# Optimization experiments

Hardware: AMD Instinct MI355X
Metric: run time of the kernel (lower is better)

Reference implementation:

```python
import jax, jax.numpy as jnp
import numpy as np
import math

V = 32000      # vocab_size
D = 1024       # hidden_dims
T_MAX = 1024   # max_txt_len
L = 4          # n_layers
H = 8          # heads (fixed in CausalMHA)
HD = D // H
B, T = 2, 1024
EPS = 1e-5


def setup_inputs() -> dict:
    key = jax.random.key(0)
    ks = jax.random.split(key, 20)
    s = 0.02
    inp = {
        "x": jax.random.randint(ks[0], (B, T), 0, V, dtype=jnp.int64) if jax.config.read("jax_enable_x64") else jax.random.randint(ks[0], (B, T), 0, V, dtype=jnp.int32),
        "tok_emb": jax.random.normal(ks[1], (V, D), jnp.float32) * s,
        "pos_emb": jax.random.normal(ks[2], (1, T_MAX, D), jnp.float32) * s,
        "ln1_g": jnp.ones((L, D), jnp.float32),
        "ln1_b": jnp.zeros((L, D), jnp.float32),
        "wqkv": jax.random.normal(ks[3], (L, D, 3 * D), jnp.float32) * s,
        "bqkv": jnp.zeros((L, 3 * D), jnp.float32),
        "wo": jax.random.normal(ks[4], (L, D, D), jnp.float32) * s,
        "bo": jnp.zeros((L, D), jnp.float32),
        "ln2_g": jnp.ones((L, D), jnp.float32),
        "ln2_b": jnp.zeros((L, D), jnp.float32),
        "wfc": jax.random.normal(ks[5], (L, D, 4 * D), jnp.float32) * s,   # no bias
        "wfc2": jax.random.normal(ks[6], (L, 4 * D, D), jnp.float32) * s,  # no bias
        "fn_g": jnp.ones((D,), jnp.float32),
        "fn_b": jnp.zeros((D,), jnp.float32),
        "wout": jax.random.normal(ks[7], (D, V), jnp.float32) * s,
        "bout": jnp.zeros((V,), jnp.float32),
    }
    return inp


def _ln(x, g, b):
    mu = jnp.mean(x, axis=-1, keepdims=True)
    var = jnp.var(x, axis=-1, keepdims=True)
    return (x - mu) * jax.lax.rsqrt(var + EPS) * g + b


def _attn(xn, wqkv_l, bqkv_l, wo_l, bo_l):
    Bb, Tt, _ = xn.shape
    qkv = xn @ wqkv_l + bqkv_l                      # [B,T,3D]
    q, k, v = jnp.split(qkv, 3, axis=-1)
    q = q.reshape(Bb, Tt, H, HD)
    k = k.reshape(Bb, Tt, H, HD)
    v = v.reshape(Bb, Tt, H, HD)
    scores = jnp.einsum("bqhd,bkhd->bhqk", q, k) / math.sqrt(HD)
    mask = jnp.triu(jnp.ones((Tt, Tt), bool), k=1)   # True above diagonal
    scores = jnp.where(mask, jnp.float32(-jnp.inf), scores)
    att = jax.nn.softmax(scores, axis=-1)
    out = jnp.einsum("bhqk,bkhd->bqhd", att, v).reshape(Bb, Tt, D)
    return out @ wo_l + bo_l


def reference(x, tok_emb, pos_emb, ln1_g, ln1_b, wqkv, bqkv, wo, bo,
              ln2_g, ln2_b, wfc, wfc2, fn_g, fn_b, wout, bout):
    Tt = x.shape[1]
    h = tok_emb[x] + pos_emb[:, :Tt, :]              # [B,T,D]
    for i in range(L):
        h = h + _attn(_ln(h, ln1_g[i], ln1_b[i]), wqkv[i], bqkv[i], wo[i], bo[i])
        hn = _ln(h, ln2_g[i], ln2_b[i])
        h = h + jax.nn.gelu(hn @ wfc[i], approximate=False) @ wfc2[i]
    h = _ln(h, fn_g, fn_b)
    return h @ wout + bout                           # [B,T,V] logits
```

## Files before the change

### kernel.cpp

```cpp
#include <hip/hip_runtime.h>
#include <math.h>
#include <stdint.h>

#define D_  1024
#define T_  1024
#define H_  8
#define HD_ 128
#define L_  4
#define V_  32000
#define M_  2048

typedef __attribute__((ext_vector_type(4))) float f32x4;
typedef __attribute__((ext_vector_type(4))) short s16x4;
typedef __attribute__((ext_vector_type(8))) short s16x8;
typedef unsigned short u16;

__device__ __forceinline__ u16 f2bf(float f) {
  union { float f; uint32_t u; } c; c.f = f;
  uint32_t r = c.u + 0x7fffu + ((c.u >> 16) & 1u);
  return (u16)(r >> 16);
}
__device__ __forceinline__ float bf2f(u16 h) {
  union { uint32_t u; float f; } c; c.u = ((uint32_t)h) << 16;
  return c.f;
}
__device__ __forceinline__ float gelu_f(float x) {
  return 0.5f * x * (1.0f + erff(x * 0.70710678118654752f));
}

__device__ __forceinline__ void gload16(const u16* g, u16* l) {
  __builtin_amdgcn_global_load_lds(
      (const __attribute__((address_space(1))) void*)(uintptr_t)g,
      (__attribute__((address_space(3))) void*)(uint32_t)(uintptr_t)l,
      16, 0, 0);
}

__device__ __forceinline__ void convT_f32_tile(const float* __restrict__ in,
                                               u16* __restrict__ out,
                                               int ldin, int ldout,
                                               int c0, int r0,
                                               u16 (*tile)[72])
{
  const int t = threadIdx.x;
  const int rr = t >> 2, cs = (t & 3) << 4;
  u16 tmp[16];
  const float* p = in + (size_t)(r0 + rr) * ldin + c0 + cs;
#pragma unroll
  for (int q = 0; q < 4; ++q) {
    f32x4 v = *(const f32x4*)(p + q * 4);
#pragma unroll
    for (int j = 0; j < 4; ++j) tmp[q * 4 + j] = f2bf(v[j]);
  }
  *(s16x8*)&tile[rr][cs]     = *(const s16x8*)tmp;
  *(s16x8*)&tile[rr][cs + 8] = *(const s16x8*)(tmp + 8);
  __syncthreads();
  const int cr = t >> 2, rs = (t & 3) << 4;
  u16 o[16];
#pragma unroll
  for (int j = 0; j < 16; ++j) o[j] = tile[rs + j][cr];
  u16* op = out + (size_t)(c0 + cr) * ldout + r0 + rs;
  *(s16x8*)op       = *(const s16x8*)o;
  *(s16x8*)(op + 8) = *(const s16x8*)(o + 8);
}

template<int INF32>
__global__ __launch_bounds__(256)
void convT_kernel(const void* __restrict__ inv, u16* __restrict__ out,
                  int ldin, int ldout, long inZ, long outZ)
{
  __shared__ __align__(16) u16 tile[64][72];
  const int c0 = blockIdx.x << 6, r0 = blockIdx.y << 6;
  if (INF32) {
    convT_f32_tile((const float*)inv + (size_t)blockIdx.z * inZ,
                   out + (size_t)blockIdx.z * outZ, ldin, ldout, c0, r0, tile);
    return;
  }
  const int t = threadIdx.x;
  const int rr = t >> 2, cs = (t & 3) << 4;
  const u16* in = (const u16*)inv + (size_t)blockIdx.z * inZ;
  const u16* p = in + (size_t)(r0 + rr) * ldin + c0 + cs;
  s16x8 v0 = *(const s16x8*)(p);
  s16x8 v1 = *(const s16x8*)(p + 8);
  *(s16x8*)&tile[rr][cs]     = v0;
  *(s16x8*)&tile[rr][cs + 8] = v1;
  __syncthreads();
  const int cr = t >> 2, rs = (t & 3) << 4;
  u16 o[16];
#pragma unroll
  for (int j = 0; j < 16; ++j) o[j] = tile[rs + j][cr];
  u16* op = out + (size_t)blockIdx.z * outZ + (size_t)(c0 + cr) * ldout + r0 + rs;
  *(s16x8*)op       = *(const s16x8*)o;
  *(s16x8*)(op + 8) = *(const s16x8*)(o + 8);
}

__global__ __launch_bounds__(256)
void conv4_kernel(const float* __restrict__ wqkv_l, const float* __restrict__ wo_l,
                  const float* __restrict__ wfc_l, const float* __restrict__ wfc2_l,
                  u16* __restrict__ Wq, u16* __restrict__ Wo,
                  u16* __restrict__ Wf1, u16* __restrict__ Wf2)
{
  __shared__ __align__(16) u16 tile[64][72];
  int f = blockIdx.x;
  if (f < 768) {
    convT_f32_tile(wqkv_l, Wq, 3 * D_, D_, (f % 48) << 6, (f / 48) << 6, tile);
  } else if (f < 1024) {
    f -= 768;
    convT_f32_tile(wo_l, Wo, D_, D_, (f & 15) << 6, (f >> 4) << 6, tile);
  } else if (f < 2048) {
    f -= 1024;
    convT_f32_tile(wfc_l, Wf1, 4 * D_, D_, (f & 63) << 6, (f >> 6) << 6, tile);
  } else {
    f -= 2048;
    convT_f32_tile(wfc2_l, Wf2, D_, 4 * D_, (f & 15) << 6, (f >> 4) << 6, tile);
  }
}

template<int TM, int ACT, int BIAS, int OUT>
__device__ __forceinline__
void gemm2_body(const u16* __restrict__ A, const u16* __restrict__ Bw,
                const float* __restrict__ bias, const float* __restrict__ res,
                void* __restrict__ Cv,
                int K, int lda, int ldb, int ldc, float scale,
                int bx, int by)
{
  constexpr int WN  = (TM == 128) ? 2 : 4;
  constexpr int WNW = 128 / WN;
  constexpr int NJ  = WNW / 16;
  constexpr int AR  = TM / 64;

  const int m0 = bx * TM, n0 = by * 128;
  const int ktiles = K >> 5;

  __shared__ __align__(16) u16 As[2][TM * 32];
  __shared__ __align__(16) u16 Bs[2][128 * 32];

  const int tid = threadIdx.x, lane = tid & 63, wave = tid >> 6;
  const int wm = wave / WN, wn = wave % WN;
  const int l15 = lane & 15, l4 = lane >> 4;
  const int srow = lane >> 2, scol = (lane & 3) << 3;

  f32x4 acc[4][NJ];
  const f32x4 z4 = {0.f, 0.f, 0.f, 0.f};
#pragma unroll
  for (int i = 0; i < 4; ++i)
#pragma unroll
    for (int j = 0; j < NJ; ++j) acc[i][j] = z4;

  auto stage = [&](int kt, int buf) {
    const int kc = (kt << 5) + scol;
#pragma unroll
    for (int r = 0; r < AR; ++r) {
      const int row = r * 64 + wave * 16;
      gload16(A + (size_t)(m0 + row + srow) * lda + kc, &As[buf][row * 32]);
    }
#pragma unroll
    for (int r = 0; r < 2; ++r) {
      const int row = r * 64 + wave * 16;
      gload16(Bw + (size_t)(n0 + row + srow) * ldb + kc, &Bs[buf][row * 32]);
    }
  };

  stage(0, 0);
  __syncthreads();

  for (int kt = 0; kt < ktiles; ++kt) {
    const int buf = kt & 1;
    if (kt + 1 < ktiles) stage(kt + 1, buf ^ 1);
    const u16* ap = &As[buf][(wm * 64 + l15) * 32 + (l4 << 3)];
    const u16* bp = &Bs[buf][(wn * WNW + l15) * 32 + (l4 << 3)];
    s16x8 af[4], bf[NJ];
#pragma unroll
    for (int i = 0; i < 4; ++i) af[i] = *(const s16x8*)(ap + i * (16 * 32));
#pragma unroll
    for (int j = 0; j < NJ; ++j) bf[j] = *(const s16x8*)(bp + j * (16 * 32));
#pragma unroll
    for (int i = 0; i < 4; ++i)
#pragma unroll
      for (int j = 0; j < NJ; ++j)
        acc[i][j] = __builtin_amdgcn_mfma_f32_16x16x32_bf16(af[i], bf[j], acc[i][j], 0, 0, 0);
    __syncthreads();
  }

  float* Cf = (float*)Cv;
  u16*   Ch = (u16*)Cv;
#pragma unroll
  for (int i = 0; i < 4; ++i) {
    const int row0 = m0 + wm * 64 + i * 16 + l4 * 4;
#pragma unroll
    for (int j = 0; j < NJ; ++j) {
      const int col = n0 + wn * WNW + j * 16 + l15;
      const float bv = BIAS ? bias[col] : 0.0f;
#pragma unroll
      for (int r = 0; r < 4; ++r) {
        float v = acc[i][j][r] * scale + bv;
        if (ACT) v = gelu_f(v);
        const size_t idx = (size_t)(row0 + r) * ldc + col;
        if (OUT == 0)      Ch[idx] = f2bf(v);
        else if (OUT == 1) Cf[idx] = v;
        else               Cf[idx] = v + res[idx];
      }
    }
  }
}

__device__ __forceinline__ int2 swz2d() {
  const int gx = gridDim.x, gy = gridDim.y;
  int flat = blockIdx.y * gx + blockIdx.x;
  const int nwg = gx * gy;
  int swz = (flat & 7) * (nwg >> 3) + (flat >> 3);
  return make_int2(swz % gx, swz / gx);
}

__global__ __launch_bounds__(256)
void gemm_qkv(const u16* A, const u16* Bw, const float* bias, void* Cv) {
  int2 b = swz2d();
  gemm2_body<128, 0, 1, 0>(A, Bw, bias, nullptr, Cv, D_, D_, D_, 3 * D_, 1.0f, b.x, b.y);
}
__global__ __launch_bounds__(256)
void gemm_wo(const u16* A, const u16* Bw, const float* bias, const float* res,
             void* Cv) {
  int2 b = swz2d();
  gemm2_body<64, 0, 1, 2>(A, Bw, bias, res, Cv, D_, D_, D_, D_, 1.0f, b.x, b.y);
}

template<int OUT, int ACT>
__device__ __forceinline__
void gemm8n_body(const u16* __restrict__ A, int lda,
                 const u16* __restrict__ Bw, int ldb,
                 void* __restrict__ Cv, int ldc, int bx, int by)
{
  const int m0 = bx << 8, n0 = by << 7;

  __shared__ __align__(16) u16 lds[49152];

  const int tid = threadIdx.x, lane = tid & 63, wave = tid >> 6;
  const int wm = wave >> 1, wn = wave & 1;
  const int l15 = lane & 15, l4 = lane >> 4;

  f32x4 acc[4][4];
  const f32x4 z4 = {0.f, 0.f, 0.f, 0.f};
#pragma unroll
  for (int i = 0; i < 4; ++i)
#pragma unroll
    for (int j = 0; j < 4; ++j) acc[i][j] = z4;

  auto stgA = [&](int buf, int kt, int kh) {
    kt = (kt < 15) ? kt : 15;
    const int slot = buf * 24576 + kh * 8192;
#pragma unroll
    for (int r = 0; r < 2; ++r) {
      const int u = r * 512 + (wave << 6) + lane;
      const int rw = u >> 2, ks = u & 3;
      const int ksw = ks ^ ((rw >> 1) & 3);
      gload16(A + (size_t)(m0 + rw) * lda + (kt << 6) + (kh << 5) + (ksw << 3),
              &lds[slot + r * 4096 + (wave << 9)]);
    }
  };
  auto stgB = [&](int buf, int kt, int kh) {
    kt = (kt < 15) ? kt : 15;
    const int slot = buf * 24576 + 16384 + kh * 4096;
    const int u = (wave << 6) + lane;
    const int rw = u >> 2, ks = u & 3;
    const int ksw = ks ^ ((rw >> 1) & 3);
    gload16(Bw + (size_t)(n0 + rw) * ldb + (kt << 6) + (kh << 5) + (ksw << 3),
            &lds[slot + (wave << 9)]);
  };

  s16x8 af[4], bfr[4];

#define LDABN(bb, kk)                                                         \
  {                                                                           \
    _Pragma("unroll") for (int f = 0; f < 4; ++f) {                           \
      const int rw = wm * 64 + f * 16 + l15;                                  \
      af[f] = *(const s16x8*)&lds[(bb) + (kk) * 8192 + rw * 32 +              \
                                  ((l4 ^ ((rw >> 1) & 3)) << 3)];             \
    }                                                                         \
    _Pragma("unroll") for (int f = 0; f < 4; ++f) {                           \
      const int rn = wn * 64 + f * 16 + l15;                                  \
      bfr[f] = *(const s16x8*)&lds[(bb) + 16384 + (kk) * 4096 + rn * 32 +     \
                                   ((l4 ^ ((rn >> 1) & 3)) << 3)];            \
    }                                                                         \
  }
#define MFMAN()                                                               \
  {                                                                           \
    __builtin_amdgcn_s_barrier();                                             \
    asm volatile("s_waitcnt lgkmcnt(0)" ::: "memory");                        \
    __builtin_amdgcn_sched_barrier(0);                                        \
    __builtin_amdgcn_s_setprio(1);                                            \
    _Pragma("unroll") for (int f = 0; f < 4; ++f)                             \
      _Pragma("unroll") for (int nf = 0; nf < 4; ++nf)                        \
        acc[f][nf] = __builtin_amdgcn_mfma_f32_16x16x32_bf16(                 \
            af[f], bfr[nf], acc[f][nf], 0, 0, 0);                             \
    __builtin_amdgcn_s_setprio(0);                                            \
  }
#define BARN() __builtin_amdgcn_s_barrier()
#define VM6()  asm volatile("s_waitcnt vmcnt(6)" ::: "memory")

  stgA(0, 0, 0); stgB(0, 0, 0);
  stgA(0, 0, 1); stgB(0, 0, 1);
  stgA(1, 1, 0); stgB(1, 1, 0);
  VM6();
  BARN();

  for (int i = 0; i < 8; ++i) {
    const int t = 2 * i;
    LDABN(0, 0);
    stgA(1, t + 1, 1); stgB(1, t + 1, 1);
    MFMAN(); VM6(); BARN();
    LDABN(0, 1);
    stgA(0, t + 2, 0); stgB(0, t + 2, 0);
    MFMAN(); VM6(); BARN();
    LDABN(24576, 0);
    stgA(0, t + 2, 1); stgB(0, t + 2, 1);
    MFMAN(); VM6(); BARN();
    LDABN(24576, 1);
    stgA(1, t + 3, 0); stgB(1, t + 3, 0);
    MFMAN(); VM6(); BARN();
  }
#undef LDABN
#undef MFMAN
#undef BARN
#undef VM6

  float* Cf = (float*)Cv;
  u16*   Ch = (u16*)Cv;
#pragma unroll
  for (int mf = 0; mf < 4; ++mf) {
    const int row0 = m0 + wm * 64 + mf * 16 + l4 * 4;
#pragma unroll
    for (int nf = 0; nf < 4; ++nf) {
      const int col = n0 + wn * 64 + nf * 16 + l15;
#pragma unroll
      for (int r = 0; r < 4; ++r) {
        float v = acc[mf][nf][r];
        if (ACT) v = gelu_f(v);
        const size_t idx = (size_t)(row0 + r) * ldc + col;
        if (OUT == 0) Ch[idx] = f2bf(v);
        else          Cf[idx] = v;
      }
    }
  }
}

__global__ __launch_bounds__(512, 1)
void gemm8n_fc1(const u16* A, const u16* Bw, void* Cv) {
  int flat = blockIdx.x;
  int swz = (flat & 7) * 32 + (flat >> 3);
  gemm8n_body<0, 1>(A, 1024, Bw, 1024, Cv, 4096, swz & 7, swz >> 3);
}
__global__ __launch_bounds__(512, 1)
void gemm8n_fc2(const u16* A, const u16* Bw, float* P) {
  int flat = blockIdx.x;
  int swz = (flat & 7) * 32 + (flat >> 3);
  const int bx = swz & 7, by = (swz >> 3) & 7, z = swz >> 6;
  gemm8n_body<1, 0>(A + z * 1024, 4096, Bw + z * 1024, 4096,
                    P + (size_t)z * M_ * D_, 1024, bx, by);
}

__global__ __launch_bounds__(512, 2)
void gemm8_logits(const u16* __restrict__ A, const u16* __restrict__ Bw,
                  const float* __restrict__ bias, float* __restrict__ C)
{
  int flat = blockIdx.x;
  int swz = (flat & 7) * 125 + (flat >> 3);
  const int bx = swz & 7;
  const int by = swz >> 3;
  const int m0 = bx << 8, n0 = by << 8;

  __shared__ __align__(16) u16 lds[65536];

  const int tid = threadIdx.x, lane = tid & 63, wave = tid >> 6;
  const int wm = wave >> 2, wn = wave & 3;
  const int l15 = lane & 15, l4 = lane >> 4;

  f32x4 acc[8][4];
  const f32x4 z4 = {0.f, 0.f, 0.f, 0.f};
#pragma unroll
  for (int i = 0; i < 8; ++i)
#pragma unroll
    for (int j = 0; j < 4; ++j) acc[i][j] = z4;

  auto stg = [&](const u16* G, int rowbase, int slot, int kt, int kh) {
    kt = (kt < 15) ? kt : 15;
#pragma unroll
    for (int r = 0; r < 2; ++r) {
      const int u = r * 512 + (wave << 6) + lane;
      const int rw = u >> 2, ks = u & 3;
      const int ksw = ks ^ ((rw >> 1) & 3);
      const u16* src = G + (size_t)(rowbase + rw) * 1024 + (kt << 6) + (kh << 5) + (ksw << 3);
      gload16(src, &lds[slot + r * 4096 + (wave << 9)]);
    }
  };

  s16x8 af[4], bfr[4];

#define LDA4(bb, kk, mh)                                                      \
  {                                                                           \
    _Pragma("unroll") for (int f = 0; f < 4; ++f) {                           \
      const int rw = wm * 128 + (mh) * 64 + f * 16 + l15;                     \
      af[f] = *(const s16x8*)&lds[(bb) + (kk) * 8192 + rw * 32 +              \
                                  ((l4 ^ ((rw >> 1) & 3)) << 3)];             \
    }                                                                         \
  }
#define LDB4(bb, kk)                                                          \
  {                                                                           \
    _Pragma("unroll") for (int f = 0; f < 4; ++f) {                           \
      const int rn = wn * 64 + f * 16 + l15;                                  \
      bfr[f] = *(const s16x8*)&lds[(bb) + 16384 + (kk) * 8192 + rn * 32 +     \
                                   ((l4 ^ ((rn >> 1) & 3)) << 3)];            \
    }                                                                         \
  }
#define MFMA16(mh)                                                            \
  {                                                                           \
    __builtin_amdgcn_s_barrier();                                             \
    asm volatile("s_waitcnt lgkmcnt(0)" ::: "memory");                        \
    __builtin_amdgcn_sched_barrier(0);                                        \
    __builtin_amdgcn_s_setprio(1);                                            \
    _Pragma("unroll") for (int f = 0; f < 4; ++f)                             \
      _Pragma("unroll") for (int nf = 0; nf < 4; ++nf)                        \
        acc[(mh) * 4 + f][nf] = __builtin_amdgcn_mfma_f32_16x16x32_bf16(      \
            af[f], bfr[nf], acc[(mh) * 4 + f][nf], 0, 0, 0);                  \
    __builtin_amdgcn_s_setprio(0);                                            \
  }
#define BAR() __builtin_amdgcn_s_barrier()
#define VM4() asm volatile("s_waitcnt vmcnt(4)" ::: "memory")

  stg(A,  m0, 0,             0, 0);
  stg(Bw, n0, 16384,         0, 0);
  stg(A,  m0, 8192,          0, 1);
  stg(Bw, n0, 16384 + 8192,  0, 1);
  stg(A,  m0, 32768,         1, 0);
  stg(Bw, n0, 32768 + 16384, 1, 0);
  VM4();
  BAR();

  for (int i = 0; i < 8; ++i) {
    const int t = 2 * i;
    LDA4(0, 0, 0); LDB4(0, 0);
    stg(A, m0, 32768 + 8192, t + 1, 1);
    MFMA16(0); BAR();
    LDA4(0, 0, 1);
    stg(Bw, n0, 32768 + 24576, t + 1, 1);
    MFMA16(1); BAR();
    LDA4(0, 1, 0); LDB4(0, 1);
    stg(A, m0, 0, t + 2, 0);
    MFMA16(0); BAR();
    LDA4(0, 1, 1);
    stg(Bw, n0, 16384, t + 2, 0);
    MFMA16(1); VM4(); BAR();
    LDA4(32768, 0, 0); LDB4(32768, 0);
    stg(A, m0, 8192, t + 2, 1);
    MFMA16(0); BAR();
    LDA4(32768, 0, 1);
    stg(Bw, n0, 16384 + 8192, t + 2, 1);
    MFMA16(1); BAR();
    LDA4(32768, 1, 0); LDB4(32768, 1);
    stg(A, m0, 32768, t + 3, 0);
    MFMA16(0); BAR();
    LDA4(32768, 1, 1);
    stg(Bw, n0, 32768 + 16384, t + 3, 0);
    MFMA16(1); VM4(); BAR();
  }
#undef LDA4
#undef LDB4
#undef MFMA16
#undef BAR
#undef VM4

  float bv[4];
#pragma unroll
  for (int nf = 0; nf < 4; ++nf) bv[nf] = bias[n0 + wn * 64 + nf * 16 + l15];
#pragma unroll
  for (int mf = 0; mf < 8; ++mf) {
    const int row0 = m0 + wm * 128 + mf * 16 + l4 * 4;
#pragma unroll
    for (int nf = 0; nf < 4; ++nf) {
      const int col = n0 + wn * 64 + nf * 16 + l15;
#pragma unroll
      for (int r = 0; r < 4; ++r)
        C[(size_t)(row0 + r) * V_ + col] = acc[mf][nf][r] + bv[nf];
    }
  }
}

__global__ __launch_bounds__(256)
void flash_attn(const u16* __restrict__ qkv, const u16* __restrict__ Vt,
                u16* __restrict__ xo)
{
  const int qb = 15 - blockIdx.x;
  const int z  = blockIdx.y;
  const int b  = z >> 3, hh = z & 7;

  __shared__ __align__(16) u16 Ks[64 * 128];
  __shared__ __align__(16) u16 Vs[128 * 64];
  __shared__ __align__(16) u16 Ps[64 * 80];

  const int tid = threadIdx.x, lane = tid & 63, w = tid >> 6;
  const int l15 = lane & 15, l4 = lane >> 4;
  const float iscale = 0.08838834764831845f;

  const int qrow = qb * 64 + w * 16 + l15;
  const u16* qptr = qkv + ((size_t)(b * T_) + qrow) * (3 * D_) + hh * HD_;

  s16x8 bQ[4];
#pragma unroll
  for (int ks = 0; ks < 4; ++ks)
    bQ[ks] = *(const s16x8*)(qptr + ks * 32 + l4 * 8);

  f32x4 O[8];
#pragma unroll
  for (int i = 0; i < 8; ++i) O[i] = {0.f, 0.f, 0.f, 0.f};
  float m_run = -1e30f, l_run = 0.f;

  const int ntiles = qb + 1;
  for (int kt = 0; kt < ntiles; ++kt) {
    __syncthreads();
    {
      const int r = tid >> 2, c = (tid & 3) << 5;
      const u16* src = qkv + ((size_t)(b * T_) + kt * 64 + r) * (3 * D_) + D_ + hh * HD_ + c;
#pragma unroll
      for (int u = 0; u < 4; ++u) {
        s16x8 v = *(const s16x8*)(src + u * 8);
        const int dblk = (c >> 3) + u;
        *(s16x8*)&Ks[r * 128 + ((dblk ^ (r & 7)) << 3)] = v;
      }
      const int d = tid >> 1, kc0 = (tid & 1) << 5;
      const u16* vsrc = Vt + ((size_t)z * HD_ + d) * T_ + kt * 64 + kc0;
#pragma unroll
      for (int u = 0; u < 4; ++u) {
        s16x8 v = *(const s16x8*)(vsrc + u * 8);
        const int kblk = (kc0 >> 3) + u;
        *(s16x8*)&Vs[d * 64 + ((kblk ^ (d & 7)) << 3)] = v;
      }
    }
    __syncthreads();

    f32x4 st[4];
#pragma unroll
    for (int mf = 0; mf < 4; ++mf) st[mf] = {0.f, 0.f, 0.f, 0.f};
#pragma unroll
    for (int ks = 0; ks < 4; ++ks) {
      s16x8 aK[4];
#pragma unroll
      for (int mf = 0; mf < 4; ++mf) {
        const int r = mf * 16 + l15;
        aK[mf] = *(const s16x8*)&Ks[r * 128 + ((((ks << 2) + l4) ^ (r & 7)) << 3)];
      }
#pragma unroll
      for (int mf = 0; mf < 4; ++mf)
        st[mf] = __builtin_amdgcn_mfma_f32_16x16x32_bf16(aK[mf], bQ[ks], st[mf], 0, 0, 0);
    }

    const bool diag = (kt == qb);
    float sv[16];
    float mx = -1e30f;
#pragma unroll
    for (int mf = 0; mf < 4; ++mf)
#pragma unroll
      for (int r = 0; r < 4; ++r) {
        float s = st[mf][r] * iscale;
        if (diag) {
          const int k = kt * 64 + mf * 16 + l4 * 4 + r;
          if (k > qrow) s = -1e30f;
        }
        sv[mf * 4 + r] = s;
        mx = fmaxf(mx, s);
      }
    mx = fmaxf(mx, __shfl_xor(mx, 16));
    mx = fmaxf(mx, __shfl_xor(mx, 32));
    const float m_new = fmaxf(m_run, mx);
    const float sc_old = __expf(m_run - m_new);
    float psum = 0.f;
    u16 pb[16];
#pragma unroll
    for (int j = 0; j < 16; ++j) {
      const float p = __expf(sv[j] - m_new);
      psum += p;
      pb[j] = f2bf(p);
    }
    psum += __shfl_xor(psum, 16);
    psum += __shfl_xor(psum, 32);
    l_run = l_run * sc_old + psum;
    m_run = m_new;

    float scr[4];
#pragma unroll
    for (int r = 0; r < 4; ++r) scr[r] = __shfl(sc_old, l4 * 4 + r);
#pragma unroll
    for (int df = 0; df < 8; ++df)
#pragma unroll
      for (int r = 0; r < 4; ++r) O[df][r] *= scr[r];

    {
      const int row = w * 16 + l15;
#pragma unroll
      for (int j = 0; j < 16; ++j) {
        const int k = (j >> 2) * 16 + l4 * 4 + (j & 3);
        Ps[row * 80 + (((k >> 3) ^ (l15 & 7)) << 3) + (k & 7)] = pb[j];
      }
    }

#pragma unroll
    for (int kc = 0; kc < 2; ++kc) {
      const int prow = w * 16 + l15;
      s16x8 aP = *(const s16x8*)&Ps[prow * 80 + ((((kc << 2) + l4) ^ (l15 & 7)) << 3)];
#pragma unroll
      for (int df = 0; df < 8; ++df) {
        const int d = df * 16 + l15;
        s16x8 bV = *(const s16x8*)&Vs[d * 64 + ((((kc << 2) + l4) ^ (d & 7)) << 3)];
        O[df] = __builtin_amdgcn_mfma_f32_16x16x32_bf16(aP, bV, O[df], 0, 0, 0);
      }
    }
  }

  const float inv_l = 1.0f / l_run;
  float invr[4];
#pragma unroll
  for (int r = 0; r < 4; ++r) invr[r] = __shfl(inv_l, l4 * 4 + r);
#pragma unroll
  for (int df = 0; df < 8; ++df)
#pragma unroll
    for (int r = 0; r < 4; ++r) {
      const int row = qb * 64 + w * 16 + l4 * 4 + r;
      xo[((size_t)(b * T_) + row) * D_ + hh * HD_ + df * 16 + l15] =
          f2bf(O[df][r] * invr[r]);
    }
}

__global__ __launch_bounds__(256)
void ln_red(float* __restrict__ hbuf, const float* __restrict__ P,
            const float* __restrict__ g, const float* __restrict__ b,
            u16* __restrict__ y, int red)
{
  __shared__ float red_s[8];
  const int row = blockIdx.x, tid = threadIdx.x;
  const size_t i = (size_t)row * D_ + tid * 4;
  f32x4 v = *(const f32x4*)&hbuf[i];
  if (red) {
#pragma unroll
    for (int zp = 0; zp < 4; ++zp) {
      f32x4 p = *(const f32x4*)&P[(size_t)zp * M_ * D_ + i];
      v[0] += p[0]; v[1] += p[1]; v[2] += p[2]; v[3] += p[3];
    }
    *(f32x4*)&hbuf[i] = v;
  }
  float s  = v[0] + v[1] + v[2] + v[3];
  float s2 = v[0]*v[0] + v[1]*v[1] + v[2]*v[2] + v[3]*v[3];
#pragma unroll
  for (int off = 32; off > 0; off >>= 1) {
    s  += __shfl_xor(s, off);
    s2 += __shfl_xor(s2, off);
  }
  if ((tid & 63) == 0) { red_s[tid >> 6] = s; red_s[4 + (tid >> 6)] = s2; }
  __syncthreads();
  s  = red_s[0] + red_s[1] + red_s[2] + red_s[3];
  s2 = red_s[4] + red_s[5] + red_s[6] + red_s[7];
  const float mean = s * (1.0f / D_);
  const float var  = s2 * (1.0f / D_) - mean * mean;
  const float rs   = rsqrtf(var + 1e-5f);
  f32x4 gg = *(const f32x4*)&g[tid * 4];
  f32x4 bb = *(const f32x4*)&b[tid * 4];
  u16 o[4];
#pragma unroll
  for (int j = 0; j < 4; ++j) o[j] = f2bf((v[j] - mean) * rs * gg[j] + bb[j]);
  *(s16x4*)&y[i] = *(const s16x4*)o;
}

__global__ __launch_bounds__(256)
void embed_kernel(const int* __restrict__ x, const float* __restrict__ tok,
                  const float* __restrict__ pos, float* __restrict__ h)
{
  const int row = blockIdx.x, tid = threadIdx.x;
  const int t = row & (T_ - 1);
  const int id = x[row];
  f32x4 a = *(const f32x4*)&tok[(size_t)id * D_ + tid * 4];
  f32x4 p = *(const f32x4*)&pos[(size_t)t * D_ + tid * 4];
  f32x4 o = {a[0] + p[0], a[1] + p[1], a[2] + p[2], a[3] + p[3]};
  *(f32x4*)&h[(size_t)row * D_ + tid * 4] = o;
}

extern "C" void kernel_launch(void* const* d_in, const int* in_sizes, int n_in,
                              void* d_out, int out_size, void* d_ws, size_t ws_size,
                              hipStream_t stream)
{
  (void)in_sizes; (void)n_in; (void)out_size; (void)ws_size;
  const int*   x     = (const int*)  d_in[0];
  const float* tok   = (const float*)d_in[1];
  const float* pos   = (const float*)d_in[2];
  const float* ln1_g = (const float*)d_in[3];
  const float* ln1_b = (const float*)d_in[4];
  const float* wqkv  = (const float*)d_in[5];
  const float* bqkv  = (const float*)d_in[6];
  const float* wo    = (const float*)d_in[7];
  const float* bo    = (const float*)d_in[8];
  const float* ln2_g = (const float*)d_in[9];
  const float* ln2_b = (const float*)d_in[10];
  const float* wfc   = (const float*)d_in[11];
  const float* wfc2  = (const float*)d_in[12];
  const float* fn_g  = (const float*)d_in[13];
  const float* fn_b  = (const float*)d_in[14];
  const float* wout  = (const float*)d_in[15];
  const float* bout  = (const float*)d_in[16];
  float* out = (float*)d_out;

  float* h  = (float*)d_ws;
  u16* xn   = (u16*)(h + (size_t)M_ * D_);
  u16* Wq   = xn  + (size_t)M_ * D_;
  u16* Wo   = Wq  + (size_t)3 * D_ * D_;
  u16* Wf1  = Wo  + (size_t)D_ * D_;
  u16* Wf2  = Wf1 + (size_t)4 * D_ * D_;
  u16* qkv  = Wf2 + (size_t)4 * D_ * D_;
  u16* Vt   = qkv + (size_t)M_ * 3 * D_;
  u16* S    = Vt  + (size_t)2 * T_ * D_;
  float* P  = (float*)(S + (size_t)M_ * 4 * D_);
  u16* WoutT = Wq;

  embed_kernel<<<M_, 256, 0, stream>>>(x, tok, pos, h);

  for (int l = 0; l < L_; ++l) {
    conv4_kernel<<<3072, 256, 0, stream>>>(
        wqkv + (size_t)l * D_ * 3 * D_, wo + (size_t)l * D_ * D_,
        wfc + (size_t)l * D_ * 4 * D_, wfc2 + (size_t)l * 4 * D_ * D_,
        Wq, Wo, Wf1, Wf2);

    ln_red<<<M_, 256, 0, stream>>>(h, P, ln1_g + l * D_, ln1_b + l * D_, xn,
                                   l > 0 ? 1 : 0);
    gemm_qkv<<<dim3(16, 24), 256, 0, stream>>>(xn, Wq, bqkv + l * 3 * D_, qkv);
    convT_kernel<0><<<dim3(16, 16, 2), 256, 0, stream>>>(
        qkv + 2 * D_, Vt, 3 * D_, T_, (long)T_ * 3 * D_, (long)T_ * D_);
    flash_attn<<<dim3(16, 16), 256, 0, stream>>>(qkv, Vt, xn);
    gemm_wo<<<dim3(32, 8), 256, 0, stream>>>(xn, Wo, bo + l * D_, h, h);
    ln_red<<<M_, 256, 0, stream>>>(h, P, ln2_g + l * D_, ln2_b + l * D_, xn, 0);
    gemm8n_fc1<<<256, 512, 0, stream>>>(xn, Wf1, S);
    gemm8n_fc2<<<256, 512, 0, stream>>>(S, Wf2, P);
  }

  ln_red<<<M_, 256, 0, stream>>>(h, P, fn_g, fn_b, xn, 1);
  convT_kernel<1><<<dim3(500, 16, 1), 256, 0, stream>>>(
      wout, WoutT, V_, D_, 0, 0);
  gemm8_logits<<<1000, 512, 0, stream>>>(xn, WoutT, bout, out);
}
```

Before: 895.1 us.

## Fuse layernorm into weight-conversion launches and halve flash-attention query tiles

New measurement: 880.8 us. About the same (-1.6%).

```diff
diff --git a/kernel.cpp b/kernel.cpp
--- a/kernel.cpp
+++ b/kernel.cpp
@@ -63,22 +63,53 @@
   *(s16x8*)(op + 8) = *(const s16x8*)(o + 8);
 }
 
-template<int INF32>
+__device__ __forceinline__
+void ln_row_body(int row, float* __restrict__ hbuf, const float* __restrict__ P,
+                 const float* __restrict__ g, const float* __restrict__ b,
+                 u16* __restrict__ y, int red, float* red_s)
+{
+  const int tid = threadIdx.x;
+  const size_t i = (size_t)row * D_ + tid * 4;
+  f32x4 v = *(const f32x4*)&hbuf[i];
+  if (red) {
+#pragma unroll
+    for (int zp = 0; zp < 4; ++zp) {
+      f32x4 p = *(const f32x4*)&P[(size_t)zp * M_ * D_ + i];
+      v[0] += p[0]; v[1] += p[1]; v[2] += p[2]; v[3] += p[3];
+    }
+    *(f32x4*)&hbuf[i] = v;
+  }
+  float s  = v[0] + v[1] + v[2] + v[3];
+  float s2 = v[0]*v[0] + v[1]*v[1] + v[2]*v[2] + v[3]*v[3];
+#pragma unroll
+  for (int off = 32; off > 0; off >>= 1) {
+    s  += __shfl_xor(s, off);
+    s2 += __shfl_xor(s2, off);
+  }
+  if ((tid & 63) == 0) { red_s[tid >> 6] = s; red_s[4 + (tid >> 6)] = s2; }
+  __syncthreads();
+  s  = red_s[0] + red_s[1] + red_s[2] + red_s[3];
+  s2 = red_s[4] + red_s[5] + red_s[6] + red_s[7];
+  const float mean = s * (1.0f / D_);
+  const float var  = s2 * (1.0f / D_) - mean * mean;
+  const float rs   = rsqrtf(var + 1e-5f);
+  f32x4 gg = *(const f32x4*)&g[tid * 4];
+  f32x4 bb = *(const f32x4*)&b[tid * 4];
+  u16 o[4];
+#pragma unroll
+  for (int j = 0; j < 4; ++j) o[j] = f2bf((v[j] - mean) * rs * gg[j] + bb[j]);
+  *(s16x4*)&y[i] = *(const s16x4*)o;
+}
+
 __global__ __launch_bounds__(256)
-void convT_kernel(const void* __restrict__ inv, u16* __restrict__ out,
-                  int ldin, int ldout, long inZ, long outZ)
+void convT_bf16(const u16* __restrict__ in, u16* __restrict__ out,
+                int ldin, int ldout, long inZ, long outZ)
 {
   __shared__ __align__(16) u16 tile[64][72];
   const int c0 = blockIdx.x << 6, r0 = blockIdx.y << 6;
-  if (INF32) {
-    convT_f32_tile((const float*)inv + (size_t)blockIdx.z * inZ,
-                   out + (size_t)blockIdx.z * outZ, ldin, ldout, c0, r0, tile);
-    return;
-  }
   const int t = threadIdx.x;
   const int rr = t >> 2, cs = (t & 3) << 4;
-  const u16* in = (const u16*)inv + (size_t)blockIdx.z * inZ;
-  const u16* p = in + (size_t)(r0 + rr) * ldin + c0 + cs;
+  const u16* p = in + (size_t)blockIdx.z * inZ + (size_t)(r0 + rr) * ldin + c0 + cs;
   s16x8 v0 = *(const s16x8*)(p);
   s16x8 v1 = *(const s16x8*)(p + 8);
   *(s16x8*)&tile[rr][cs]     = v0;
@@ -94,13 +125,18 @@
 }
 
 __global__ __launch_bounds__(256)
-void conv4_kernel(const float* __restrict__ wqkv_l, const float* __restrict__ wo_l,
-                  const float* __restrict__ wfc_l, const float* __restrict__ wfc2_l,
-                  u16* __restrict__ Wq, u16* __restrict__ Wo,
-                  u16* __restrict__ Wf1, u16* __restrict__ Wf2)
+void conv4ln_kernel(const float* __restrict__ wqkv_l, const float* __restrict__ wo_l,
+                    const float* __restrict__ wfc_l, const float* __restrict__ wfc2_l,
+                    u16* __restrict__ Wq, u16* __restrict__ Wo,
+                    u16* __restrict__ Wf1, u16* __restrict__ Wf2,
+                    float* __restrict__ hbuf, const float* __restrict__ P,
+                    const float* __restrict__ g, const float* __restrict__ b,
+                    u16* __restrict__ y, int red)
 {
   __shared__ __align__(16) u16 tile[64][72];
   int f = blockIdx.x;
+  if (f < 2048) { ln_row_body(f, hbuf, P, g, b, y, red, (float*)tile); return; }
+  f -= 2048;
   if (f < 768) {
     convT_f32_tile(wqkv_l, Wq, 3 * D_, D_, (f % 48) << 6, (f / 48) << 6, tile);
   } else if (f < 1024) {
@@ -113,6 +149,19 @@
     f -= 2048;
     convT_f32_tile(wfc2_l, Wf2, D_, 4 * D_, (f & 15) << 6, (f >> 4) << 6, tile);
   }
+}
+
+__global__ __launch_bounds__(256)
+void convwout_ln(const float* __restrict__ wout, u16* __restrict__ WoutT,
+                 float* __restrict__ hbuf, const float* __restrict__ P,
+                 const float* __restrict__ g, const float* __restrict__ b,
+                 u16* __restrict__ y)
+{
+  __shared__ __align__(16) u16 tile[64][72];
+  int f = blockIdx.x;
+  if (f < 2048) { ln_row_body(f, hbuf, P, g, b, y, 1, (float*)tile); return; }
+  f -= 2048;
+  convT_f32_tile(wout, WoutT, V_, D_, (f % 500) << 6, (f / 500) << 6, tile);
 }
 
 template<int TM, int ACT, int BIAS, int OUT>
@@ -483,23 +532,25 @@
   }
 }
 
-__global__ __launch_bounds__(256)
+__global__ __launch_bounds__(128)
 void flash_attn(const u16* __restrict__ qkv, const u16* __restrict__ Vt,
                 u16* __restrict__ xo)
 {
-  const int qb = 15 - blockIdx.x;
-  const int z  = blockIdx.y;
+  int flat = blockIdx.x;
+  int swz = (flat & 7) * 64 + (flat >> 3);
+  const int qb = 31 - (swz & 31);
+  const int z  = swz >> 5;
   const int b  = z >> 3, hh = z & 7;
 
   __shared__ __align__(16) u16 Ks[64 * 128];
   __shared__ __align__(16) u16 Vs[128 * 64];
-  __shared__ __align__(16) u16 Ps[64 * 80];
+  __shared__ __align__(16) u16 Ps[32 * 80];
 
   const int tid = threadIdx.x, lane = tid & 63, w = tid >> 6;
   const int l15 = lane & 15, l4 = lane >> 4;
   const float iscale = 0.08838834764831845f;
 
-  const int qrow = qb * 64 + w * 16 + l15;
+  const int qrow = qb * 32 + w * 16 + l15;
   const u16* qptr = qkv + ((size_t)(b * T_) + qrow) * (3 * D_) + hh * HD_;
 
   s16x8 bQ[4];
@@ -512,25 +563,24 @@
   for (int i = 0; i < 8; ++i) O[i] = {0.f, 0.f, 0.f, 0.f};
   float m_run = -1e30f, l_run = 0.f;
 
-  const int ntiles = qb + 1;
+  const int ntiles = (qb >> 1) + 1;
   for (int kt = 0; kt < ntiles; ++kt) {
     __syncthreads();
     {
-      const int r = tid >> 2, c = (tid & 3) << 5;
-      const u16* src = qkv + ((size_t)(b * T_) + kt * 64 + r) * (3 * D_) + D_ + hh * HD_ + c;
-#pragma unroll
-      for (int u = 0; u < 4; ++u) {
+      const int r = tid >> 1, c0 = (tid & 1) << 6;
+      const u16* src = qkv + ((size_t)(b * T_) + kt * 64 + r) * (3 * D_) + D_ + hh * HD_ + c0;
+#pragma unroll
+      for (int u = 0; u < 8; ++u) {
         s16x8 v = *(const s16x8*)(src + u * 8);
-        const int dblk = (c >> 3) + u;
+        const int dblk = (c0 >> 3) + u;
         *(s16x8*)&Ks[r * 128 + ((dblk ^ (r & 7)) << 3)] = v;
       }
-      const int d = tid >> 1, kc0 = (tid & 1) << 5;
-      const u16* vsrc = Vt + ((size_t)z * HD_ + d) * T_ + kt * 64 + kc0;
-#pragma unroll
-      for (int u = 0; u < 4; ++u) {
+      const int d = tid;
+      const u16* vsrc = Vt + ((size_t)z * HD_ + d) * T_ + kt * 64;
+#pragma unroll
+      for (int u = 0; u < 8; ++u) {
         s16x8 v = *(const s16x8*)(vsrc + u * 8);
-        const int kblk = (kc0 >> 3) + u;
-        *(s16x8*)&Vs[d * 64 + ((kblk ^ (d & 7)) << 3)] = v;
+        *(s16x8*)&Vs[d * 64 + ((u ^ (d & 7)) << 3)] = v;
       }
     }
     __syncthreads();
@@ -551,7 +601,7 @@
         st[mf] = __builtin_amdgcn_mfma_f32_16x16x32_bf16(aK[mf], bQ[ks], st[mf], 0, 0, 0);
     }
 
-    const bool diag = (kt == qb);
+    const bool diag = (kt == ntiles - 1);
     float sv[16];
     float mx = -1e30f;
 #pragma unroll
@@ -621,49 +671,18 @@
   for (int df = 0; df < 8; ++df)
 #pragma unroll
     for (int r = 0; r < 4; ++r) {
-      const int row = qb * 64 + w * 16 + l4 * 4 + r;
+      const int row = qb * 32 + w * 16 + l4 * 4 + r;
       xo[((size_t)(b * T_) + row) * D_ + hh * HD_ + df * 16 + l15] =
           f2bf(O[df][r] * invr[r]);
     }
 }
 
 __global__ __launch_bounds__(256)
-void ln_red(float* __restrict__ hbuf, const float* __restrict__ P,
-            const float* __restrict__ g, const float* __restrict__ b,
-            u16* __restrict__ y, int red)
+void ln_bf16(const float* __restrict__ x, const float* __restrict__ g,
+             const float* __restrict__ b, u16* __restrict__ y)
 {
   __shared__ float red_s[8];
-  const int row = blockIdx.x, tid = threadIdx.x;
-  const size_t i = (size_t)row * D_ + tid * 4;
-  f32x4 v = *(const f32x4*)&hbuf[i];
-  if (red) {
-#pragma unroll
-    for (int zp = 0; zp < 4; ++zp) {
-      f32x4 p = *(const f32x4*)&P[(size_t)zp * M_ * D_ + i];
-      v[0] += p[0]; v[1] += p[1]; v[2] += p[2]; v[3] += p[3];
-    }
-    *(f32x4*)&hbuf[i] = v;
-  }
-  float s  = v[0] + v[1] + v[2] + v[3];
-  float s2 = v[0]*v[0] + v[1]*v[1] + v[2]*v[2] + v[3]*v[3];
-#pragma unroll
-  for (int off = 32; off > 0; off >>= 1) {
-    s  += __shfl_xor(s, off);
-    s2 += __shfl_xor(s2, off);
-  }
-  if ((tid & 63) == 0) { red_s[tid >> 6] = s; red_s[4 + (tid >> 6)] = s2; }
-  __syncthreads();
-  s  = red_s[0] + red_s[1] + red_s[2] + red_s[3];
-  s2 = red_s[4] + red_s[5] + red_s[6] + red_s[7];
-  const float mean = s * (1.0f / D_);
-  const float var  = s2 * (1.0f / D_) - mean * mean;
-  const float rs   = rsqrtf(var + 1e-5f);
-  f32x4 gg = *(const f32x4*)&g[tid * 4];
-  f32x4 bb = *(const f32x4*)&b[tid * 4];
-  u16 o[4];
-#pragma unroll
-  for (int j = 0; j < 4; ++j) o[j] = f2bf((v[j] - mean) * rs * gg[j] + bb[j]);
-  *(s16x4*)&y[i] = *(const s16x4*)o;
+  ln_row_body(blockIdx.x, (float*)x, nullptr, g, b, y, 0, red_s);
 }
 
 __global__ __launch_bounds__(256)
@@ -718,25 +737,21 @@
   embed_kernel<<<M_, 256, 0, stream>>>(x, tok, pos, h);
 
   for (int l = 0; l < L_; ++l) {
-    conv4_kernel<<<3072, 256, 0, stream>>>(
+    conv4ln_kernel<<<5120, 256, 0, stream>>>(
         wqkv + (size_t)l * D_ * 3 * D_, wo + (size_t)l * D_ * D_,
         wfc + (size_t)l * D_ * 4 * D_, wfc2 + (size_t)l * 4 * D_ * D_,
-        Wq, Wo, Wf1, Wf2);
-
-    ln_red<<<M_, 256, 0, stream>>>(h, P, ln1_g + l * D_, ln1_b + l * D_, xn,
-                                   l > 0 ? 1 : 0);
+        Wq, Wo, Wf1, Wf2,
+        h, P, ln1_g + l * D_, ln1_b + l * D_, xn, l > 0 ? 1 : 0);
     gemm_qkv<<<dim3(16, 24), 256, 0, stream>>>(xn, Wq, bqkv + l * 3 * D_, qkv);
-    convT_kernel<0><<<dim3(16, 16, 2), 256, 0, stream>>>(
+    convT_bf16<<<dim3(16, 16, 2), 256, 0, stream>>>(
         qkv + 2 * D_, Vt, 3 * D_, T_, (long)T_ * 3 * D_, (long)T_ * D_);
-    flash_attn<<<dim3(16, 16), 256, 0, stream>>>(qkv, Vt, xn);
+    flash_attn<<<512, 128, 0, stream>>>(qkv, Vt, xn);
     gemm_wo<<<dim3(32, 8), 256, 0, stream>>>(xn, Wo, bo + l * D_, h, h);
-    ln_red<<<M_, 256, 0, stream>>>(h, P, ln2_g + l * D_, ln2_b + l * D_, xn, 0);
+    ln_bf16<<<M_, 256, 0, stream>>>(h, ln2_g + l * D_, ln2_b + l * D_, xn);
     gemm8n_fc1<<<256, 512, 0, stream>>>(xn, Wf1, S);
     gemm8n_fc2<<<256, 512, 0, stream>>>(S, Wf2, P);
   }
 
-  ln_red<<<M_, 256, 0, stream>>>(h, P, fn_g, fn_b, xn, 1);
-  convT_kernel<1><<<dim3(500, 16, 1), 256, 0, stream>>>(
-      wout, WoutT, V_, D_, 0, 0);
+  convwout_ln<<<10048, 256, 0, stream>>>(wout, WoutT, h, P, fn_g, fn_b, xn);
   gemm8_logits<<<1000, 512, 0, stream>>>(xn, WoutT, bout, out);
 }
```
